# Optimization experiments

Measured on AMD Instinct MI355X. Metric: run time of the kernel, lower is better.

## Reference

```python
import jax, jax.numpy as jnp
import numpy as np

# Larq ste_sign: forward sign(x) with sign(0)=+1; backward is identity clipped to |x|<=1 (STE).
@jax.custom_vjp
def ste_sign(x):
    return jnp.where(x >= 0, jnp.ones((), x.dtype), -jnp.ones((), x.dtype))

def _ste_fwd(x):
    return ste_sign(x), x

def _ste_bwd(x, g):
    return (g * (jnp.abs(x) <= 1).astype(g.dtype),)

ste_sign.defvjp(_ste_fwd, _ste_bwd)


def setup_inputs() -> dict:
    key = jax.random.key(0)
    k1, k2 = jax.random.split(key)
    x = jax.random.normal(k1, (16, 112, 112, 256), dtype=jnp.float32)      # NHWC
    kernel = jax.random.normal(k2, (3, 3, 256, 1), dtype=jnp.float32) * 0.1  # (kh, kw, C, mult)
    return {"x": x, "kernel": kernel}


def reference(x, kernel):
    # Quantize input and depthwise kernel, then standard depthwise conv (stride 1, SAME, no bias).
    xq = ste_sign(x)
    kq = ste_sign(kernel)
    kh, kw, C, mult = kernel.shape
    rhs = kq.reshape(kh, kw, 1, C * mult)  # HWIO layout for grouped conv
    out = jax.lax.conv_general_dilated(
        xq, rhs,
        window_strides=(1, 1),
        padding="SAME",
        feature_group_count=C,
        dimension_numbers=("NHWC", "HWIO", "NHWC"),
    )
    return out
```

## Files before the change

### kernel.cpp

```cpp
#include <hip/hip_runtime.h>


constexpr int N = 16, H = 112, W = 112, C = 256;
constexpr int TW = 14;
constexpr int COLS = TW + 2;
constexpr int RW = 4;

typedef float f32x4 __attribute__((ext_vector_type(4)));

struct TrueT  { static constexpr bool value = true;  };
struct FalseT { static constexpr bool value = false; };

__global__ __launch_bounds__(256, 4) void bsign_dw3x3_lds(
        const float* __restrict__ x, const float* __restrict__ k,
        float* __restrict__ out) {
    __shared__ unsigned sig[COLS * C];

    const int lane = threadIdx.x & 63;
    const int wq   = threadIdx.x >> 6;
    const int c0   = lane << 2;
    const int h0   = blockIdx.y * 16;
    const int w0   = blockIdx.x * TW;
    const int n    = blockIdx.z;

    unsigned k3[3][4] = {{0,0,0,0},{0,0,0,0},{0,0,0,0}};
#pragma unroll
    for (int t = 0; t < 9; ++t) {
        const uint4 kv = *reinterpret_cast<const uint4*>(k + t * C + c0);
        const int kr = t / 3, kj = t % 3;
        k3[kj][0] |= (kv.x >> 31) << kr;
        k3[kj][1] |= (kv.y >> 31) << kr;
        k3[kj][2] |= (kv.z >> 31) << kr;
        k3[kj][3] |= (kv.w >> 31) << kr;
    }

    const size_t rowstride = (size_t)W * C;

    const bool ptop = (h0 > 0);
    const bool pbot = (h0 + 16 < H);
#pragma unroll
    for (int q = 0; q < 4; ++q) {
        const int ci   = (wq << 2) + q;
        const int xcol = w0 - 1 + ci;
        unsigned s0 = 0, s1 = 0, s2 = 0, s3 = 0;
        if (xcol >= 0 && xcol < W) {
            const float* cp = x + (size_t)(n * H + h0 - 1) * rowstride
                                + (size_t)xcol * C + c0;
#pragma unroll
            for (int p = 0; p < 18; ++p) {
                if (p == 0  && !ptop) continue;
                if (p == 17 && !pbot) continue;
                const uint4 v = *reinterpret_cast<const uint4*>(
                    cp + (size_t)p * rowstride);
                s0 |= (v.x >> 31) << p;
                s1 |= (v.y >> 31) << p;
                s2 |= (v.z >> 31) << p;
                s3 |= (v.w >> 31) << p;
            }
        }
        uint4 sv; sv.x = s0; sv.y = s1; sv.z = s2; sv.w = s3;
        *reinterpret_cast<uint4*>(&sig[ci * C + c0]) = sv;
    }
    __syncthreads();

    const int hbase = h0 + (wq << 2);
    unsigned bm[RW]; int nrr[RW];
#pragma unroll
    for (int r = 0; r < RW; ++r) {
        const int h = hbase + r;
        unsigned b = 7u;
        if (h == 0)     b &= ~1u;
        if (h == H - 1) b &= ~4u;
        bm[r]  = b;
        nrr[r] = (b == 7u) ? 3 : 2;
    }
    const int sh0 = wq << 2;
    float* obase = out + (size_t)(n * H + hbase) * rowstride
                       + (size_t)w0 * C + c0;

    unsigned m2[4], m1[4], cc[4];
    auto ldsig = [&](int ci, unsigned d[4]) {
        const uint4 v = *reinterpret_cast<const uint4*>(&sig[ci * C + c0]);
        d[0] = v.x >> sh0; d[1] = v.y >> sh0;
        d[2] = v.z >> sh0; d[3] = v.w >> sh0;
    };
    auto emit = [&](int wo, const unsigned a[4], const unsigned bc[4],
                    const unsigned ce[4], auto jt0, auto jt2) {
        constexpr int NT = (decltype(jt0)::value ? 1 : 0) + 1
                         + (decltype(jt2)::value ? 1 : 0);
        float* orow = obase + (size_t)wo * C;
#pragma unroll
        for (int r = 0; r < RW; ++r) {
            const unsigned b = bm[r];
            int n0 = 0, n1 = 0, n2 = 0, n3 = 0;
            auto term = [&](const unsigned s[4], const unsigned kk[4]) {
                n0 += __popc(((s[0] >> r) ^ kk[0]) & b);
                n1 += __popc(((s[1] >> r) ^ kk[1]) & b);
                n2 += __popc(((s[2] >> r) ^ kk[2]) & b);
                n3 += __popc(((s[3] >> r) ^ kk[3]) & b);
            };
            if constexpr (decltype(jt0)::value) term(a, k3[0]);
            term(bc, k3[1]);
            if constexpr (decltype(jt2)::value) term(ce, k3[2]);
            const int nt = NT * nrr[r];
            f32x4 ov;
            ov[0] = (float)(nt - 2 * n0);
            ov[1] = (float)(nt - 2 * n1);
            ov[2] = (float)(nt - 2 * n2);
            ov[3] = (float)(nt - 2 * n3);
            __builtin_nontemporal_store(ov,
                reinterpret_cast<f32x4*>(orow + (size_t)r * rowstride));
        }
    };

    ldsig(0, m2); ldsig(1, m1); ldsig(2, cc);
    if (w0 > 0) emit(0, m2, m1, cc, TrueT{},  TrueT{});
    else        emit(0, m2, m1, cc, FalseT{}, TrueT{});
#pragma unroll
    for (int ch = 0; ch < 4; ++ch) { m2[ch] = m1[ch]; m1[ch] = cc[ch]; }

#pragma unroll
    for (int wo = 1; wo < TW - 1; ++wo) {
        ldsig(wo + 2, cc);
        emit(wo, m2, m1, cc, TrueT{}, TrueT{});
#pragma unroll
        for (int ch = 0; ch < 4; ++ch) { m2[ch] = m1[ch]; m1[ch] = cc[ch]; }
    }

    ldsig(TW + 1, cc);
    if (w0 + TW < W) emit(TW - 1, m2, m1, cc, TrueT{}, TrueT{});
    else             emit(TW - 1, m2, m1, cc, TrueT{}, FalseT{});
}

extern "C" void kernel_launch(void* const* d_in, const int* in_sizes, int n_in,
                              void* d_out, int out_size, void* d_ws, size_t ws_size,
                              hipStream_t stream) {
    const float* x = (const float*)d_in[0];
    const float* k = (const float*)d_in[1];
    float* out = (float*)d_out;

    dim3 grid(W / TW, H / 16, N);
    bsign_dw3x3_lds<<<grid, 256, 0, stream>>>(x, k, out);
}
```

Measured before the change: 359.3 us.

## Interleave column loads across rows and stream output rows with per-column partial sums

The global load loop is reordered so each thread issues its four column loads per input row together, which exposes more independent memory requests in flight. Kernel sign packing moves after the loads. The compute phase now iterates per output row, computing the three kernel-column partial sums for each LDS column once and sliding them along the width. Each output row is then written as a contiguous stream. This trades the old column-major emit, which wrote four rows per column, for row-contiguous stores, at the cost of more LDS reads.

```diff
diff --git a/kernel.cpp b/kernel.cpp
--- a/kernel.cpp
+++ b/kernel.cpp
@@ -8,10 +8,7 @@
 
 typedef float f32x4 __attribute__((ext_vector_type(4)));
 
-struct TrueT  { static constexpr bool value = true;  };
-struct FalseT { static constexpr bool value = false; };
-
-__global__ __launch_bounds__(256, 4) void bsign_dw3x3_lds(
+__global__ __launch_bounds__(256, 4) void bsign_dw3x3_rowstream(
         const float* __restrict__ x, const float* __restrict__ k,
         float* __restrict__ out) {
     __shared__ unsigned sig[COLS * C];
@@ -23,6 +20,43 @@
     const int w0   = blockIdx.x * TW;
     const int n    = blockIdx.z;
 
+    const size_t rowstride = (size_t)W * C;
+    const bool ptop = (h0 > 0);
+    const bool pbot = (h0 + 16 < H);
+
+    const int ciB = wq << 2;
+    const float* xbase = x + (size_t)(n * H + h0 - 1) * rowstride + c0;
+    bool cv[4];
+    const float* cp[4];
+#pragma unroll
+    for (int q = 0; q < 4; ++q) {
+        const int xc = w0 - 1 + ciB + q;
+        cv[q] = (xc >= 0 && xc < W);
+        cp[q] = xbase + (ptrdiff_t)xc * (ptrdiff_t)C;
+    }
+    unsigned sq[4][4] = {{0,0,0,0},{0,0,0,0},{0,0,0,0},{0,0,0,0}};
+#pragma unroll
+    for (int p = 0; p < 18; ++p) {
+        if (p == 0  && !ptop) continue;
+        if (p == 17 && !pbot) continue;
+        const size_t ro = (size_t)p * rowstride;
+#pragma unroll
+        for (int q = 0; q < 4; ++q) {
+            if (cv[q]) {
+                const uint4 v = *reinterpret_cast<const uint4*>(cp[q] + ro);
+                sq[q][0] |= (v.x >> 31) << p;
+                sq[q][1] |= (v.y >> 31) << p;
+                sq[q][2] |= (v.z >> 31) << p;
+                sq[q][3] |= (v.w >> 31) << p;
+            }
+        }
+    }
+#pragma unroll
+    for (int q = 0; q < 4; ++q) {
+        uint4 sv; sv.x = sq[q][0]; sv.y = sq[q][1]; sv.z = sq[q][2]; sv.w = sq[q][3];
+        *reinterpret_cast<uint4*>(&sig[(ciB + q) * C + c0]) = sv;
+    }
+
     unsigned k3[3][4] = {{0,0,0,0},{0,0,0,0},{0,0,0,0}};
 #pragma unroll
     for (int t = 0; t < 9; ++t) {
@@ -33,103 +67,66 @@
         k3[kj][2] |= (kv.z >> 31) << kr;
         k3[kj][3] |= (kv.w >> 31) << kr;
     }
-
-    const size_t rowstride = (size_t)W * C;
-
-    const bool ptop = (h0 > 0);
-    const bool pbot = (h0 + 16 < H);
-#pragma unroll
-    for (int q = 0; q < 4; ++q) {
-        const int ci   = (wq << 2) + q;
-        const int xcol = w0 - 1 + ci;
-        unsigned s0 = 0, s1 = 0, s2 = 0, s3 = 0;
-        if (xcol >= 0 && xcol < W) {
-            const float* cp = x + (size_t)(n * H + h0 - 1) * rowstride
-                                + (size_t)xcol * C + c0;
-#pragma unroll
-            for (int p = 0; p < 18; ++p) {
-                if (p == 0  && !ptop) continue;
-                if (p == 17 && !pbot) continue;
-                const uint4 v = *reinterpret_cast<const uint4*>(
-                    cp + (size_t)p * rowstride);
-                s0 |= (v.x >> 31) << p;
-                s1 |= (v.y >> 31) << p;
-                s2 |= (v.z >> 31) << p;
-                s3 |= (v.w >> 31) << p;
-            }
-        }
-        uint4 sv; sv.x = s0; sv.y = s1; sv.z = s2; sv.w = s3;
-        *reinterpret_cast<uint4*>(&sig[ci * C + c0]) = sv;
-    }
     __syncthreads();
 
     const int hbase = h0 + (wq << 2);
-    unsigned bm[RW]; int nrr[RW];
+    float* obase = out + (size_t)(n * H + hbase) * rowstride
+                       + (size_t)w0 * C + c0;
+    const bool ledge = (w0 == 0), redge = (w0 + TW == W);
+
 #pragma unroll
     for (int r = 0; r < RW; ++r) {
-        const int h = hbase + r;
-        unsigned b = 7u;
-        if (h == 0)     b &= ~1u;
-        if (h == H - 1) b &= ~4u;
-        bm[r]  = b;
-        nrr[r] = (b == 7u) ? 3 : 2;
-    }
-    const int sh0 = wq << 2;
-    float* obase = out + (size_t)(n * H + hbase) * rowstride
-                       + (size_t)w0 * C + c0;
+        const int h  = hbase + r;
+        const unsigned b = (h == 0) ? 6u : (h == H - 1) ? 3u : 7u;
+        const int nr = (h == 0 || h == H - 1) ? 2 : 3;
+        const int sh = (wq << 2) + r;
+        float* orow = obase + (size_t)r * rowstride;
 
-    unsigned m2[4], m1[4], cc[4];
-    auto ldsig = [&](int ci, unsigned d[4]) {
-        const uint4 v = *reinterpret_cast<const uint4*>(&sig[ci * C + c0]);
-        d[0] = v.x >> sh0; d[1] = v.y >> sh0;
-        d[2] = v.z >> sh0; d[3] = v.w >> sh0;
-    };
-    auto emit = [&](int wo, const unsigned a[4], const unsigned bc[4],
-                    const unsigned ce[4], auto jt0, auto jt2) {
-        constexpr int NT = (decltype(jt0)::value ? 1 : 0) + 1
-                         + (decltype(jt2)::value ? 1 : 0);
-        float* orow = obase + (size_t)wo * C;
+        int t0m2[4], t0m1[4], t1m1[4], tj0[4], tj1[4], tj2[4];
+
+        auto tcol = [&](int ci) {
+            const uint4 v = *reinterpret_cast<const uint4*>(&sig[ci * C + c0]);
+            const unsigned d[4] = {v.x >> sh, v.y >> sh, v.z >> sh, v.w >> sh};
 #pragma unroll
-        for (int r = 0; r < RW; ++r) {
-            const unsigned b = bm[r];
-            int n0 = 0, n1 = 0, n2 = 0, n3 = 0;
-            auto term = [&](const unsigned s[4], const unsigned kk[4]) {
-                n0 += __popc(((s[0] >> r) ^ kk[0]) & b);
-                n1 += __popc(((s[1] >> r) ^ kk[1]) & b);
-                n2 += __popc(((s[2] >> r) ^ kk[2]) & b);
-                n3 += __popc(((s[3] >> r) ^ kk[3]) & b);
-            };
-            if constexpr (decltype(jt0)::value) term(a, k3[0]);
-            term(bc, k3[1]);
-            if constexpr (decltype(jt2)::value) term(ce, k3[2]);
-            const int nt = NT * nrr[r];
-            f32x4 ov;
-            ov[0] = (float)(nt - 2 * n0);
-            ov[1] = (float)(nt - 2 * n1);
-            ov[2] = (float)(nt - 2 * n2);
-            ov[3] = (float)(nt - 2 * n3);
-            __builtin_nontemporal_store(ov,
-                reinterpret_cast<f32x4*>(orow + (size_t)r * rowstride));
+            for (int ch = 0; ch < 4; ++ch) {
+                tj0[ch] = nr - 2 * __popc((d[ch] ^ k3[0][ch]) & b);
+                tj1[ch] = nr - 2 * __popc((d[ch] ^ k3[1][ch]) & b);
+                tj2[ch] = nr - 2 * __popc((d[ch] ^ k3[2][ch]) & b);
+            }
+        };
+
+        if (ledge) {
+#pragma unroll
+            for (int ch = 0; ch < 4; ++ch) t0m2[ch] = 0;
+        } else {
+            tcol(0);
+#pragma unroll
+            for (int ch = 0; ch < 4; ++ch) t0m2[ch] = tj0[ch];
         }
-    };
-
-    ldsig(0, m2); ldsig(1, m1); ldsig(2, cc);
-    if (w0 > 0) emit(0, m2, m1, cc, TrueT{},  TrueT{});
-    else        emit(0, m2, m1, cc, FalseT{}, TrueT{});
+        tcol(1);
 #pragma unroll
-    for (int ch = 0; ch < 4; ++ch) { m2[ch] = m1[ch]; m1[ch] = cc[ch]; }
+        for (int ch = 0; ch < 4; ++ch) { t0m1[ch] = tj0[ch]; t1m1[ch] = tj1[ch]; }
 
 #pragma unroll
-    for (int wo = 1; wo < TW - 1; ++wo) {
-        ldsig(wo + 2, cc);
-        emit(wo, m2, m1, cc, TrueT{}, TrueT{});
+        for (int ci = 2; ci < COLS; ++ci) {
+            if (ci == COLS - 1 && redge) {
 #pragma unroll
-        for (int ch = 0; ch < 4; ++ch) { m2[ch] = m1[ch]; m1[ch] = cc[ch]; }
+                for (int ch = 0; ch < 4; ++ch) tj2[ch] = 0;
+            } else {
+                tcol(ci);
+            }
+            f32x4 ov;
+#pragma unroll
+            for (int ch = 0; ch < 4; ++ch)
+                ov[ch] = (float)(t0m2[ch] + t1m1[ch] + tj2[ch]);
+            __builtin_nontemporal_store(ov,
+                reinterpret_cast<f32x4*>(orow + (size_t)(ci - 2) * C));
+#pragma unroll
+            for (int ch = 0; ch < 4; ++ch) {
+                t0m2[ch] = t0m1[ch]; t0m1[ch] = tj0[ch]; t1m1[ch] = tj1[ch];
+            }
+        }
     }
-
-    ldsig(TW + 1, cc);
-    if (w0 + TW < W) emit(TW - 1, m2, m1, cc, TrueT{}, TrueT{});
-    else             emit(TW - 1, m2, m1, cc, TrueT{}, FalseT{});
 }
 
 extern "C" void kernel_launch(void* const* d_in, const int* in_sizes, int n_in,
@@ -140,5 +137,5 @@
     float* out = (float*)d_out;
 
     dim3 grid(W / TW, H / 16, N);
-    bsign_dw3x3_lds<<<grid, 256, 0, stream>>>(x, k, out);
+    bsign_dw3x3_rowstream<<<grid, 256, 0, stream>>>(x, k, out);
 }
```

New measurement: 356.9 us. Within noise of the previous version (-0.7%).
